# Kernel optimization log

Hardware: AMD Instinct MI355X
Metric: run time of the kernel (lower is better)

## Reference

```python
import jax, jax.numpy as jnp
import numpy as np

# Config mirrors init_kwargs
B = 8            # batch_size
L = 1024         # new tokens per sequence (prefill)
BS = 16          # block_size
MAXB = 128       # max_blocks_per_seq = ceil(2048/16)
H = 8            # num_kv_heads
D = 128          # head_dim
NLAYERS = 2
TOTAL = B * MAXB * NLAYERS  # 2048 total blocks


def setup_inputs() -> dict:
    key = jax.random.key(0)
    k1, k2 = jax.random.split(key)
    return {
        "layer_idx": 0,
        "key_states": jax.random.normal(k1, (B * L, H, D), jnp.float32),
        "value_states": jax.random.normal(k2, (B * L, H, D), jnp.float32),
        "input_len": jnp.full((B,), L, jnp.int32),
        "cu_seqlens": (jnp.arange(B + 1, dtype=jnp.int32) * L),
        "k_cache": jnp.zeros((TOTAL, H, BS, D), jnp.float32),
        "v_cache": jnp.zeros((TOTAL, H, BS, D), jnp.float32),
        "block_tables": jnp.zeros((B, MAXB), jnp.int32),  # layer slice
        "seq_lens": jnp.zeros((B,), jnp.int32),           # layer slice
        "free_blocks": jnp.arange(TOTAL, dtype=jnp.int32),
    }


def reference(layer_idx, key_states, value_states, input_len, cu_seqlens,
              k_cache, v_cache, block_tables, seq_lens, free_blocks):
    # ---- block allocation (vectorized form of the per-sequence python loop) ----
    old_nb = (seq_lens + BS - 1) // BS                 # blocks already held
    new_nb = (seq_lens + input_len + BS - 1) // BS     # blocks needed
    alloc = new_nb - old_nb                            # per-seq new blocks
    cum = jnp.cumsum(alloc)                            # tail-pop order: seq i gets
    num_free = free_blocks.shape[0]                    # free_blocks[num_free-cum[i] : ...]
    start = num_free - cum                             # [B]
    slots = jnp.arange(MAXB, dtype=jnp.int32)[None, :]                  # [1, MAXB]
    valid = (slots >= old_nb[:, None]) & (slots < new_nb[:, None])      # [B, MAXB]
    free_idx = jnp.clip(start[:, None] + (slots - old_nb[:, None]), 0, num_free - 1)
    bt = jnp.where(valid, free_blocks[free_idx], block_tables)          # updated table

    # ---- scatter new K/V tokens into paged cache (store_paged_kv) ----
    # assumes uniform input_len == L (as built in setup_inputs)
    t = jnp.arange(L, dtype=jnp.int32)[None, :]        # [1, L]
    tok_idx = cu_seqlens[:B][:, None] + t              # [B, L] index into packed K/V
    pos = seq_lens[:, None] + t                        # absolute position in sequence
    blk = jnp.take_along_axis(bt, pos // BS, axis=1)   # [B, L] physical block id
    off = pos % BS                                     # [B, L] offset within block

    keys = key_states[tok_idx.ravel()]                 # [B*L, H, D]
    vals = value_states[tok_idx.ravel()]
    k_new = k_cache.at[blk.ravel(), :, off.ravel(), :].set(keys)
    v_new = v_cache.at[blk.ravel(), :, off.ravel(), :].set(vals)
    return jnp.stack([k_new, v_new])  # [2, TOTAL, H, BS, D]
```

## Files before the change

### kernel.cpp

```cpp
#include <hip/hip_runtime.h>

constexpr int B     = 8;
constexpr int L     = 1024;
constexpr int BS    = 16;
constexpr int MAXB  = 128;
constexpr int H     = 8;
constexpr int D     = 128;
constexpr int TOTAL = 2048;
constexpr int CACHE_ELEMS = TOTAL * H * BS * D;

typedef float f4 __attribute__((ext_vector_type(4)));

__global__ __launch_bounds__(256, 8) void fused_gather_kernel(
        const f4* __restrict__ key_states,
        const f4* __restrict__ value_states,
        const f4* __restrict__ k_cache,
        const f4* __restrict__ v_cache,
        const int* __restrict__ input_len,
        const int* __restrict__ cu_seqlens,
        const int* __restrict__ seq_lens,
        const int* __restrict__ block_tables,
        const int* __restrict__ free_blocks,
        f4*        __restrict__ out) {
    constexpr int C4   = CACHE_ELEMS / 4;
    constexpr int PB4  = H * BS * D / 4;
    constexpr int CH   = 8;
    constexpr int WG4  = 256 * CH;

    const int tid  = threadIdx.x;
    const int base = blockIdx.x * WG4 + tid;

    const int c    = base >= C4 ? 1 : 0;
    const int rel0 = base - c * C4;
    const int blk  = rel0 >> 12;

    __shared__ int sm;
    if (tid == 0) sm = -1;
    __syncthreads();

    int cum = 0;
    #pragma unroll
    for (int b = 0; b < B; ++b) {
        const int sl    = seq_lens[b];
        const int il    = input_len[b];
        const int oldb  = (sl + BS - 1) / BS;
        const int newb  = (sl + il + BS - 1) / BS;
        cum += newb - oldb;
        const int startb = TOTAL - cum;
        for (int j = sl / BS + tid; j < newb; j += 256) {
            int cand;
            if (j >= oldb) {
                int fi = startb + (j - oldb);
                fi = min(max(fi, 0), TOTAL - 1);
                cand = free_blocks[fi];
            } else {
                cand = block_tables[b * MAXB + j];
            }
            if (cand == blk) sm = (b << 20) | j;
        }
    }
    __syncthreads();
    const int m = sm;

    const f4* __restrict__ cache = c ? v_cache : k_cache;

    f4 vals[CH];
    if (m >= 0) {
        const int b    = m >> 20;
        const int j    = m & 0xFFFFF;
        const int sl   = seq_lens[b];
        const int il   = input_len[b];
        const int tok0 = cu_seqlens[b] - sl;
        const f4* __restrict__ src = c ? value_states : key_states;
        #pragma unroll
        for (int k = 0; k < CH; ++k) {
            const int rel4 = rel0 + k * 256;
            const int r    = rel4 & (PB4 - 1);
            const int h    = r >> 9;
            const int off  = (r >> 5) & 15;
            const int d4   = r & 31;
            const int pos  = j * BS + off;
            if (pos >= sl && pos < sl + il) {
                vals[k] = __builtin_nontemporal_load(
                    &src[(tok0 + pos) * (H * D / 4) + h * 32 + d4]);
            } else {
                vals[k] = __builtin_nontemporal_load(&cache[rel4]);
            }
        }
    } else {
        #pragma unroll
        for (int k = 0; k < CH; ++k)
            vals[k] = __builtin_nontemporal_load(&cache[rel0 + k * 256]);
    }

    #pragma unroll
    for (int k = 0; k < CH; ++k)
        __builtin_nontemporal_store(vals[k], &out[base + k * 256]);
}

extern "C" void kernel_launch(void* const* d_in, const int* in_sizes, int n_in,
                              void* d_out, int out_size, void* d_ws, size_t ws_size,
                              hipStream_t stream) {
    const float* key_states   = (const float*)d_in[1];
    const float* value_states = (const float*)d_in[2];
    const int*   input_len    = (const int*)d_in[3];
    const int*   cu_seqlens   = (const int*)d_in[4];
    const float* k_cache      = (const float*)d_in[5];
    const float* v_cache      = (const float*)d_in[6];
    const int*   block_tables = (const int*)d_in[7];
    const int*   seq_lens     = (const int*)d_in[8];
    const int*   free_blocks  = (const int*)d_in[9];

    constexpr int WG4    = 256 * 8;
    const int     total4 = 2 * CACHE_ELEMS / 4;
    const int     blocks = total4 / WG4;
    fused_gather_kernel<<<blocks, 256, 0, stream>>>(
        (const f4*)key_states, (const f4*)value_states,
        (const f4*)k_cache, (const f4*)v_cache,
        input_len, cu_seqlens, seq_lens, block_tables, free_blocks,
        (f4*)d_out);
}
```

Measured before the change: 464.5 us.

## Split into device memcpy of caches plus per-token scatter patch kernel

```diff
diff --git a/kernel.cpp b/kernel.cpp
--- a/kernel.cpp
+++ b/kernel.cpp
@@ -8,94 +8,69 @@
 constexpr int D     = 128;
 constexpr int TOTAL = 2048;
 constexpr int CACHE_ELEMS = TOTAL * H * BS * D;
+constexpr size_t CACHE_BYTES = (size_t)CACHE_ELEMS * 4;
 
 typedef float f4 __attribute__((ext_vector_type(4)));
 
-__global__ __launch_bounds__(256, 8) void fused_gather_kernel(
+__global__ __launch_bounds__(256) void patch_tokens_kernel(
         const f4* __restrict__ key_states,
         const f4* __restrict__ value_states,
-        const f4* __restrict__ k_cache,
-        const f4* __restrict__ v_cache,
         const int* __restrict__ input_len,
         const int* __restrict__ cu_seqlens,
         const int* __restrict__ seq_lens,
         const int* __restrict__ block_tables,
         const int* __restrict__ free_blocks,
         f4*        __restrict__ out) {
-    constexpr int C4   = CACHE_ELEMS / 4;
-    constexpr int PB4  = H * BS * D / 4;
-    constexpr int CH   = 8;
-    constexpr int WG4  = 256 * CH;
+    constexpr int C4  = CACHE_ELEMS / 4;
+    constexpr int PT4 = H * D / 4;
 
-    const int tid  = threadIdx.x;
-    const int base = blockIdx.x * WG4 + tid;
+    const int tok = blockIdx.x;
+    const int tid = threadIdx.x;
 
-    const int c    = base >= C4 ? 1 : 0;
-    const int rel0 = base - c * C4;
-    const int blk  = rel0 >> 12;
+    int b = 0;
+    #pragma unroll
+    for (int bb = 0; bb < B - 1; ++bb)
+        if (tok >= cu_seqlens[bb + 1]) b = bb + 1;
 
-    __shared__ int sm;
-    if (tid == 0) sm = -1;
-    __syncthreads();
+    const int t  = tok - cu_seqlens[b];
+    const int il = input_len[b];
+    if (t >= il) return;
 
-    int cum = 0;
+    const int sl  = seq_lens[b];
+    const int pos = sl + t;
+    const int j   = pos / BS;
+    const int off = pos % BS;
+
+    int cum = 0, oldb = 0, startb = 0;
     #pragma unroll
-    for (int b = 0; b < B; ++b) {
-        const int sl    = seq_lens[b];
-        const int il    = input_len[b];
-        const int oldb  = (sl + BS - 1) / BS;
-        const int newb  = (sl + il + BS - 1) / BS;
-        cum += newb - oldb;
-        const int startb = TOTAL - cum;
-        for (int j = sl / BS + tid; j < newb; j += 256) {
-            int cand;
-            if (j >= oldb) {
-                int fi = startb + (j - oldb);
-                fi = min(max(fi, 0), TOTAL - 1);
-                cand = free_blocks[fi];
-            } else {
-                cand = block_tables[b * MAXB + j];
-            }
-            if (cand == blk) sm = (b << 20) | j;
-        }
-    }
-    __syncthreads();
-    const int m = sm;
-
-    const f4* __restrict__ cache = c ? v_cache : k_cache;
-
-    f4 vals[CH];
-    if (m >= 0) {
-        const int b    = m >> 20;
-        const int j    = m & 0xFFFFF;
-        const int sl   = seq_lens[b];
-        const int il   = input_len[b];
-        const int tok0 = cu_seqlens[b] - sl;
-        const f4* __restrict__ src = c ? value_states : key_states;
-        #pragma unroll
-        for (int k = 0; k < CH; ++k) {
-            const int rel4 = rel0 + k * 256;
-            const int r    = rel4 & (PB4 - 1);
-            const int h    = r >> 9;
-            const int off  = (r >> 5) & 15;
-            const int d4   = r & 31;
-            const int pos  = j * BS + off;
-            if (pos >= sl && pos < sl + il) {
-                vals[k] = __builtin_nontemporal_load(
-                    &src[(tok0 + pos) * (H * D / 4) + h * 32 + d4]);
-            } else {
-                vals[k] = __builtin_nontemporal_load(&cache[rel4]);
-            }
-        }
-    } else {
-        #pragma unroll
-        for (int k = 0; k < CH; ++k)
-            vals[k] = __builtin_nontemporal_load(&cache[rel0 + k * 256]);
+    for (int bb = 0; bb <= B - 1; ++bb) {
+        if (bb > b) break;
+        const int s  = seq_lens[bb];
+        const int ob = (s + BS - 1) / BS;
+        const int nb = (s + input_len[bb] + BS - 1) / BS;
+        cum += nb - ob;
+        if (bb == b) { oldb = ob; startb = TOTAL - cum; }
     }
 
-    #pragma unroll
-    for (int k = 0; k < CH; ++k)
-        __builtin_nontemporal_store(vals[k], &out[base + k * 256]);
+    int blk;
+    if (j >= oldb) {
+        int fi = startb + (j - oldb);
+        fi = min(max(fi, 0), TOTAL - 1);
+        blk = free_blocks[fi];
+    } else {
+        blk = block_tables[b * MAXB + j];
+    }
+
+    const int h  = tid >> 5;
+    const int d4 = tid & 31;
+    const int src_idx = tok * PT4 + tid;
+    const int dst_rel = blk * (PT4 * BS) + h * (BS * D / 4) + off * (D / 4) + d4;
+
+    const f4 kv = __builtin_nontemporal_load(&key_states[src_idx]);
+    const f4 vv = __builtin_nontemporal_load(&value_states[src_idx]);
+    __builtin_amdgcn_sched_barrier(0);
+    __builtin_nontemporal_store(kv, &out[dst_rel]);
+    __builtin_nontemporal_store(vv, &out[C4 + dst_rel]);
 }
 
 extern "C" void kernel_launch(void* const* d_in, const int* in_sizes, int n_in,
@@ -111,12 +86,14 @@
     const int*   seq_lens     = (const int*)d_in[8];
     const int*   free_blocks  = (const int*)d_in[9];
 
-    constexpr int WG4    = 256 * 8;
-    const int     total4 = 2 * CACHE_ELEMS / 4;
-    const int     blocks = total4 / WG4;
-    fused_gather_kernel<<<blocks, 256, 0, stream>>>(
+    char* out_bytes = (char*)d_out;
+    hipMemcpyAsync(out_bytes,               k_cache, CACHE_BYTES,
+                   hipMemcpyDeviceToDevice, stream);
+    hipMemcpyAsync(out_bytes + CACHE_BYTES, v_cache, CACHE_BYTES,
+                   hipMemcpyDeviceToDevice, stream);
+
+    patch_tokens_kernel<<<B * L, 256, 0, stream>>>(
         (const f4*)key_states, (const f4*)value_states,
-        (const f4*)k_cache, (const f4*)v_cache,
         input_len, cu_seqlens, seq_lens, block_tables, free_blocks,
         (f4*)d_out);
 }
```

Result: slower. 489.2 us (+5.3%).
